# Optimization experiments

Hardware: AMD Instinct MI355X
Metric: run time of the kernel (lower is better)

## Reference

```python
import jax, jax.numpy as jnp
import numpy as np

B, L, D, NH, NP = 8, 4096, 384, 8, 4


def setup_inputs() -> dict:
    key = jax.random.key(0)
    ks = jax.random.split(key, 16)
    s = 1.0 / np.sqrt(D)
    f32 = jnp.float32
    inp = {
        'query': jax.random.normal(ks[0], (B, L, D), f32),
        'key':   jax.random.normal(ks[1], (B, L, D), f32),
        'value': jax.random.normal(ks[2], (B, L, D), f32),
        # linear weights stored as [in, out]; x @ W + b
        'Wq': jax.random.normal(ks[3], (D, D), f32) * s,
        'bq': jnp.zeros((D,), f32),
        'Wk': jax.random.normal(ks[4], (D, D), f32) * s,
        'bk': jnp.zeros((D,), f32),
        'Wv': jax.random.normal(ks[5], (D, D), f32) * s,
        'bv': jnp.zeros((D,), f32),
        'Woff': jax.random.normal(ks[6], (D, NH * NP * 2), f32) * s,
        'boff': jnp.zeros((NH * NP * 2,), f32),
        'Wwt': jax.random.normal(ks[7], (D, NH * NP), f32) * s,
        'bwt': jnp.zeros((NH * NP,), f32),
        'Wo': jax.random.normal(ks[8], (D, D), f32) * s,
        'bo': jnp.zeros((D,), f32),
        'num_heads': NH,
        'n_points': NP,
    }
    return inp


def reference(query, key, value, Wq, bq, Wk, bk, Wv, bv, Woff, boff, Wwt, bwt, Wo, bo, num_heads, n_points):
    Bq, Lq, Dm = query.shape
    Lk = key.shape[1]
    Lv = value.shape[1]
    hd = Dm // num_heads
    h = w = int(round(np.sqrt(Lk)))  # original: feature_size = int(sqrt(Lk))

    q = query @ Wq + bq          # computed as in original (only its reshape is used via output path)
    k = key @ Wk + bk            # faithful: k_proj is computed but unused downstream
    v = value @ Wv + bv

    # offsets [B, nH, Lq, nP, 2] and softmax point weights [B, nH, Lq, nP]
    off = (query @ Woff + boff).reshape(Bq, Lq, num_heads, n_points, 2).transpose(0, 2, 1, 3, 4)
    wt = jax.nn.softmax((query @ Wwt + bwt).reshape(Bq, Lq, num_heads, n_points).transpose(0, 2, 1, 3), axis=-1)

    # reference grid: ref[...,0] = x (tiled over rows), ref[...,1] = y (repeated over cols)
    yy = jnp.linspace(0.0, 1.0, h)
    xx = jnp.linspace(0.0, 1.0, w)
    gy, gx = jnp.meshgrid(yy, xx, indexing='ij')
    ref = jnp.stack([gx.reshape(-1), gy.reshape(-1)], axis=-1)  # [L, 2]

    loc = jnp.clip(ref[None, None, :, None, :] + off, 0.0, 1.0)  # [B,nH,Lq,nP,2]
    # NOTE: faithful to source, which multiplies component 0 by (h-1) (its 'h' coord)
    ph = loc[..., 0] * (h - 1)   # row pixel coord, in [0, h-1]
    pw = loc[..., 1] * (w - 1)   # col pixel coord, in [0, w-1]

    y0 = jnp.floor(ph)
    x0 = jnp.floor(pw)
    wy = (ph - y0)[..., None]
    wx = (pw - x0)[..., None]
    y0i = y0.astype(jnp.int32)
    x0i = x0.astype(jnp.int32)
    y1i = jnp.minimum(y0i + 1, h - 1)
    x1i = jnp.minimum(x0i + 1, w - 1)

    vh = v.reshape(Bq, Lv, num_heads, hd).transpose(0, 2, 1, 3)  # [B,nH,Lv,hd]

    def gather(yi, xi):
        idx = (yi * w + xi).reshape(Bq, num_heads, Lq * n_points, 1)
        return jnp.take_along_axis(vh, idx, axis=2).reshape(Bq, num_heads, Lq, n_points, hd)

    # bilinear sample (align_corners=True; coords in-range so zero-padding never triggers)
    sampled = ((1 - wy) * ((1 - wx) * gather(y0i, x0i) + wx * gather(y0i, x1i))
               + wy * ((1 - wx) * gather(y1i, x0i) + wx * gather(y1i, x1i)))

    out = jnp.einsum('bhlp,bhlpd->bhld', wt, sampled)  # weighted point aggregation
    out = out.transpose(0, 2, 1, 3).reshape(Bq, Lq, Dm)
    return out @ Wo + bo  # dropout is identity in eval mode
```

## Files before the change

### kernel.cpp

```cpp
#include <hip/hip_runtime.h>
#include <hip/hip_bf16.h>
#include <stdint.h>

using bf16 = __hip_bfloat16;

typedef __attribute__((ext_vector_type(8))) short short8;
typedef __attribute__((ext_vector_type(4))) float float4v;

namespace {
constexpr int kL  = 4096;
constexpr int kD  = 384;
constexpr int kGW = 64;
constexpr int kM  = 32768;
constexpr int kAP = 392;

constexpr size_t nValue = (size_t)kM * kD;
constexpr size_t nW     = (size_t)kD * kD;
constexpr size_t nWcat  = (size_t)96 * kD;

constexpr size_t oWvt  = 0;
constexpr size_t oWot  = oWvt  + nW * 2;
constexpr size_t oWch  = oWot  + nW * 2;
constexpr size_t oWcl  = oWch  + nWcat * 2;
constexpr size_t oBcat = oWcl  + nWcat * 2;
constexpr size_t oVB   = (oBcat + 96 * 4 + 255) & ~size_t(255);
constexpr size_t oProj = oVB   + nValue * 2;
}

__device__ __forceinline__ void load_lds_16(const void* g, void* l) {
  __builtin_amdgcn_global_load_lds((const __attribute__((address_space(1))) void*)g,
                                   (__attribute__((address_space(3))) void*)l,
                                   16, 0, 0);
}

__device__ __forceinline__ short bf16bits(float f) {
  bf16 h = __float2bfloat16(f);
  return *reinterpret_cast<short*>(&h);
}

__device__ __forceinline__ float bf16raw2f(unsigned short u) {
  union { unsigned int i; float f; } c;
  c.i = ((unsigned int)u) << 16;
  return c.f;
}

__device__ __forceinline__ short8 pack_hi8(const float4& f0, const float4& f1) {
  short8 hx;
  hx[0] = bf16bits(f0.x); hx[1] = bf16bits(f0.y);
  hx[2] = bf16bits(f0.z); hx[3] = bf16bits(f0.w);
  hx[4] = bf16bits(f1.x); hx[5] = bf16bits(f1.y);
  hx[6] = bf16bits(f1.z); hx[7] = bf16bits(f1.w);
  return hx;
}

__device__ __forceinline__ void pack_hilo8(const float4& f0, const float4& f1,
                                           short8& hx, short8& lx) {
  const float fv[8] = {f0.x, f0.y, f0.z, f0.w, f1.x, f1.y, f1.z, f1.w};
  #pragma unroll
  for (int q = 0; q < 8; ++q) {
    const bf16 h = __float2bfloat16(fv[q]);
    hx[q] = *reinterpret_cast<const short*>(&h);
    const bf16 lo = __float2bfloat16(fv[q] - __bfloat162float(h));
    lx[q] = *reinterpret_cast<const short*>(&lo);
  }
}

__global__ void prep_kernel(const float* __restrict__ Wv,
                            const float* __restrict__ Wo,
                            const float* __restrict__ Woff,
                            const float* __restrict__ Wwt,
                            const float* __restrict__ boff,
                            const float* __restrict__ bwt,
                            bf16* __restrict__ Wvt, bf16* __restrict__ Wot,
                            bf16* __restrict__ Wch, bf16* __restrict__ Wcl,
                            float* __restrict__ bcat)
{
  size_t i = (size_t)blockIdx.x * 256 + threadIdx.x;
  if (i < nW) {
    const int n = (int)(i / kD), k = (int)(i % kD);
    Wvt[i] = __float2bfloat16(Wv[(size_t)k * kD + n]);
    return;
  }
  i -= nW;
  if (i < nW) {
    const int n = (int)(i / kD), k = (int)(i % kD);
    Wot[i] = __float2bfloat16(Wo[(size_t)k * kD + n]);
    return;
  }
  i -= nW;
  if (i < nWcat) {
    const int n = (int)(i / kD), k = (int)(i % kD);
    const float val = (n < 64) ? Woff[(size_t)k * 64 + n] : Wwt[(size_t)k * 32 + (n - 64)];
    const bf16 h = __float2bfloat16(val);
    Wch[i] = h;
    Wcl[i] = __float2bfloat16(val - __bfloat162float(h));
    return;
  }
  i -= nWcat;
  if (i < 96) bcat[i] = (i < 64) ? boff[i] : bwt[i - 64];
}

__device__ __forceinline__
void vgemm_body(char* smem, int bid,
                const float* __restrict__ A, const bf16* __restrict__ Bt,
                const float* __restrict__ bias, bf16* __restrict__ Cout)
{
  bf16* sA = (bf16*)smem;
  char* sBB = smem + 16384;
  const int tid  = threadIdx.x;
  const int lane = tid & 63;
  const int wave = tid >> 6;
  const int bm = bid / 3, bn = bid % 3;
  const int m0 = bm * 128, n0 = bn * 128;
  const int wm = (wave >> 1) * 64, wn = (wave & 1) * 64;
  const int r16 = lane & 15, quad = lane >> 4;

  float4v acc[4][4];
  #pragma unroll
  for (int i = 0; i < 4; ++i)
    #pragma unroll
    for (int j = 0; j < 4; ++j) acc[i][j] = (float4v){0.f, 0.f, 0.f, 0.f};

  const int e0 = tid, e1 = tid + 256;
  const int rA0 = e0 >> 2, gA0 = e0 & 3;
  const int rA1 = e1 >> 2, gA1 = e1 & 3;
  const int wA0 = rA0 * 32 + (gA0 ^ ((rA0 >> 1) & 3)) * 8;
  const int wA1 = rA1 * 32 + (gA1 ^ ((rA1 >> 1) & 3)) * 8;
  const int sBc0 = (gA0 ^ ((rA0 >> 1) & 3)) * 8;
  const int sBc1 = (gA1 ^ ((rA1 >> 1) & 3)) * 8;

  float4 f00, f01, f10, f11;
  auto loadA = [&](int k0) {
    const float* s0 = A + (size_t)(m0 + rA0) * kD + k0 + gA0 * 8;
    f00 = *(const float4*)s0; f01 = *(const float4*)(s0 + 4);
    const float* s1 = A + (size_t)(m0 + rA1) * kD + k0 + gA1 * 8;
    f10 = *(const float4*)s1; f11 = *(const float4*)(s1 + 4);
  };
  auto writeA = [&](int buf) {
    *(short8*)(sA + buf * 4096 + wA0) = pack_hi8(f00, f01);
    *(short8*)(sA + buf * 4096 + wA1) = pack_hi8(f10, f11);
  };
  auto stageB = [&](int k0, int buf) {
    load_lds_16(Bt + (size_t)(n0 + rA0) * kD + k0 + sBc0, sBB + buf * 8192 + e0 * 16);
    load_lds_16(Bt + (size_t)(n0 + rA1) * kD + k0 + sBc1, sBB + buf * 8192 + e1 * 16);
  };

  loadA(0);
  stageB(0, 0);
  writeA(0);
  __syncthreads();

  for (int kt = 0; kt < 12; ++kt) {
    const int cur = kt & 1, nxt = cur ^ 1;
    if (kt < 11) {
      loadA((kt + 1) * 32);
      stageB((kt + 1) * 32, nxt);
    }
    const bf16* sAc = sA + cur * 4096;
    const bf16* sBc = (const bf16*)(sBB + cur * 8192);
    short8 av[4], bv[4];
    #pragma unroll
    for (int i = 0; i < 4; ++i) {
      const int row = wm + i * 16 + r16;
      av[i] = *(const short8*)(sAc + row * 32 + (quad ^ ((row >> 1) & 3)) * 8);
    }
    #pragma unroll
    for (int j = 0; j < 4; ++j) {
      const int row = wn + j * 16 + r16;
      bv[j] = *(const short8*)(sBc + row * 32 + (quad ^ ((row >> 1) & 3)) * 8);
    }
    #pragma unroll
    for (int i = 0; i < 4; ++i)
      #pragma unroll
      for (int j = 0; j < 4; ++j)
        acc[i][j] = __builtin_amdgcn_mfma_f32_16x16x32_bf16(av[i], bv[j], acc[i][j], 0, 0, 0);
    if (kt < 11) {
      writeA(nxt);
      __syncthreads();
    }
  }

  #pragma unroll
  for (int j = 0; j < 4; ++j) {
    const int col = n0 + wn + j * 16 + r16;
    const float bj = bias[col];
    #pragma unroll
    for (int i = 0; i < 4; ++i) {
      const int mbase = m0 + wm + i * 16 + quad * 4;
      #pragma unroll
      for (int r = 0; r < 4; ++r)
        Cout[(size_t)(mbase + r) * kD + col] = __float2bfloat16(acc[i][j][r] + bj);
    }
  }
}

__device__ __forceinline__
void proj_body(char* smem, int bid,
               const float* __restrict__ Q,
               const bf16* __restrict__ WhT, const bf16* __restrict__ WlT,
               const float* __restrict__ bc, float* __restrict__ proj)
{
  bf16* sAh = (bf16*)smem;
  bf16* sAl = (bf16*)(smem + 8192);
  bf16* sBh = (bf16*)(smem + 16384);
  bf16* sBl = (bf16*)(smem + 22528);
  const int tid  = threadIdx.x;
  const int lane = tid & 63;
  const int wave = tid >> 6;
  const int m0 = bid * 128;
  const int wm = (wave >> 1) * 64, wn = (wave & 1) * 48;
  const int r16 = lane & 15, quad = lane >> 4;

  float4v acc[4][3];
  #pragma unroll
  for (int i = 0; i < 4; ++i)
    #pragma unroll
    for (int j = 0; j < 3; ++j) acc[i][j] = (float4v){0.f, 0.f, 0.f, 0.f};

  for (int kt = 0; kt < 12; ++kt) {
    const int k0 = kt * 32;
    #pragma unroll
    for (int r = 0; r < 2; ++r) {
      const int e = tid + r * 256;
      const int row = e >> 2, j = e & 3;
      const float* src = Q + (size_t)(m0 + row) * kD + k0 + j * 8;
      const float4 f0 = *(const float4*)src;
      const float4 f1 = *(const float4*)(src + 4);
      short8 hx, lx;
      pack_hilo8(f0, f1, hx, lx);
      const int jw = j ^ ((row >> 1) & 3);
      *(short8*)(sAh + row * 32 + jw * 8) = hx;
      *(short8*)(sAl + row * 32 + jw * 8) = lx;
    }
    {
      int c = tid;
      int row = c >> 2, j = c & 3, js = j ^ ((row >> 1) & 3);
      load_lds_16(WhT + (size_t)row * kD + k0 + js * 8, (char*)sBh + c * 16);
      if (tid < 128) {
        c = tid + 256;
        row = c >> 2; j = c & 3; js = j ^ ((row >> 1) & 3);
        load_lds_16(WhT + (size_t)row * kD + k0 + js * 8, (char*)sBh + c * 16);
      } else {
        c = tid - 128;
        row = c >> 2; j = c & 3; js = j ^ ((row >> 1) & 3);
        load_lds_16(WlT + (size_t)row * kD + k0 + js * 8, (char*)sBl + c * 16);
      }
      c = tid + 128;
      row = c >> 2; j = c & 3; js = j ^ ((row >> 1) & 3);
      load_lds_16(WlT + (size_t)row * kD + k0 + js * 8, (char*)sBl + c * 16);
    }
    __syncthreads();

    short8 avh[4], avl[4];
    #pragma unroll
    for (int i = 0; i < 4; ++i) {
      const int row = wm + i * 16 + r16;
      const int ch = quad ^ ((row >> 1) & 3);
      avh[i] = *(const short8*)(sAh + row * 32 + ch * 8);
      avl[i] = *(const short8*)(sAl + row * 32 + ch * 8);
    }
    #pragma unroll
    for (int j = 0; j < 3; ++j) {
      const int row = wn + j * 16 + r16;
      const int ch = quad ^ ((row >> 1) & 3);
      const short8 bvh = *(const short8*)(sBh + row * 32 + ch * 8);
      const short8 bvl = *(const short8*)(sBl + row * 32 + ch * 8);
      #pragma unroll
      for (int i = 0; i < 4; ++i) {
        acc[i][j] = __builtin_amdgcn_mfma_f32_16x16x32_bf16(avh[i], bvh, acc[i][j], 0, 0, 0);
        acc[i][j] = __builtin_amdgcn_mfma_f32_16x16x32_bf16(avh[i], bvl, acc[i][j], 0, 0, 0);
        acc[i][j] = __builtin_amdgcn_mfma_f32_16x16x32_bf16(avl[i], bvh, acc[i][j], 0, 0, 0);
      }
    }
    __syncthreads();
  }

  #pragma unroll
  for (int j = 0; j < 3; ++j) {
    const int col = wn + j * 16 + r16;
    const float bj = bc[col];
    #pragma unroll
    for (int i = 0; i < 4; ++i) {
      const int mbase = m0 + wm + i * 16 + quad * 4;
      #pragma unroll
      for (int r = 0; r < 4; ++r)
        proj[(size_t)(mbase + r) * 96 + col] = acc[i][j][r] + bj;
    }
  }
}

__global__ __launch_bounds__(256)
void fat_kernel(const float* __restrict__ value, const bf16* __restrict__ Wvt,
                const float* __restrict__ bv,    bf16* __restrict__ vB,
                const float* __restrict__ Q,     const bf16* __restrict__ Wch,
                const bf16* __restrict__ Wcl,    const float* __restrict__ bcat,
                float* __restrict__ proj)
{
  __shared__ __align__(16) char smem[32768];
  const int pb = blockIdx.x;
  if (pb < 256) {
    proj_body(smem, pb, Q, Wch, Wcl, bcat, proj);
  } else {
    vgemm_body(smem, pb - 256, value, Wvt, bv, vB);
  }
}

__global__ __launch_bounds__(512)
void tail_kernel(const float* __restrict__ proj, const bf16* __restrict__ v,
                 const bf16* __restrict__ Wot, const float* __restrict__ bo,
                 float* __restrict__ out)
{
  __shared__ __align__(16) char smem[66560];
  bf16*   sAgg  = (bf16*)smem;
  int4*   scoff = (int4*)(smem + 50176);
  float4* scw   = (float4*)(smem + 58368);

  const int raw   = blockIdx.x;
  const int chunk = (raw & 7) * 64 + (raw >> 3);
  const int m0    = chunk * 64;
  const int b     = m0 >> 12;
  const int l0    = m0 & 4095;
  const int t     = threadIdx.x;

  for (int ct = 0; ct < 4; ++ct) {
    const int tok0 = ct * 16;
    {
      const int tl = t >> 5, pt = t & 31;
      const int tok = tok0 + tl;
      const int l   = l0 + tok;
      const float* pb_ = proj + (size_t)(m0 + tok) * 96;
      const float2 off = *(const float2*)(pb_ + 2 * pt);
      const int h = pt >> 2, p = pt & 3;
      const float4 lg = *(const float4*)(pb_ + 64 + h * 4);
      const float g[4] = {lg.x, lg.y, lg.z, lg.w};
      const float mx = fmaxf(fmaxf(g[0], g[1]), fmaxf(g[2], g[3]));
      float e[4], sum = 0.f;
      #pragma unroll
      for (int jj = 0; jj < 4; ++jj) { e[jj] = expf(g[jj] - mx); sum += e[jj]; }
      const float wt = e[p] / sum;
      const float refx = (float)(l & 63) * (1.0f / 63.0f);
      const float refy = (float)(l >> 6) * (1.0f / 63.0f);
      const float locx = fminf(fmaxf(refx + off.x, 0.f), 1.f);
      const float locy = fminf(fmaxf(refy + off.y, 0.f), 1.f);
      const float ph = locx * 63.0f;
      const float pw = locy * 63.0f;
      const float fy = floorf(ph), fx = floorf(pw);
      const int y0 = (int)fy, x0 = (int)fx;
      const int y1 = min(y0 + 1, 63), x1 = min(x0 + 1, 63);
      const float wy = ph - fy, wx = pw - fx;
      scoff[tl * 32 + pt] = make_int4((y0 * kGW + x0) * kD, (y0 * kGW + x1) * kD,
                                      (y1 * kGW + x0) * kD, (y1 * kGW + x1) * kD);
      scw[tl * 32 + pt] = make_float4(wt * (1.f - wy) * (1.f - wx), wt * (1.f - wy) * wx,
                                      wt * wy * (1.f - wx),         wt * wy * wx);
    }
    __syncthreads();
    #pragma unroll
    for (int it = 0; it < 3; ++it) {
      const int task = t + it * 512;
      const int tl = task / 96;
      const int q  = task - tl * 96;
      const int h  = q / 12;
      const int col = q * 4;
      const unsigned short* vb = (const unsigned short*)(v + (size_t)b * kL * kD + col);
      float4v acc = (float4v){0.f, 0.f, 0.f, 0.f};
      #pragma unroll
      for (int p = 0; p < 4; ++p) {
        const int4   o = scoff[tl * 32 + h * 4 + p];
        const float4 w = scw  [tl * 32 + h * 4 + p];
        const ushort4 u0 = *(const ushort4*)(vb + o.x);
        const ushort4 u1 = *(const ushort4*)(vb + o.y);
        const ushort4 u2 = *(const ushort4*)(vb + o.z);
        const ushort4 u3 = *(const ushort4*)(vb + o.w);
        acc[0] += w.x * bf16raw2f(u0.x) + w.y * bf16raw2f(u1.x)
                + w.z * bf16raw2f(u2.x) + w.w * bf16raw2f(u3.x);
        acc[1] += w.x * bf16raw2f(u0.y) + w.y * bf16raw2f(u1.y)
                + w.z * bf16raw2f(u2.y) + w.w * bf16raw2f(u3.y);
        acc[2] += w.x * bf16raw2f(u0.z) + w.y * bf16raw2f(u1.z)
                + w.z * bf16raw2f(u2.z) + w.w * bf16raw2f(u3.z);
        acc[3] += w.x * bf16raw2f(u0.w) + w.y * bf16raw2f(u1.w)
                + w.z * bf16raw2f(u2.w) + w.w * bf16raw2f(u3.w);
      }
      ushort4 ou;
      ou.x = (unsigned short)bf16bits(acc[0]);
      ou.y = (unsigned short)bf16bits(acc[1]);
      ou.z = (unsigned short)bf16bits(acc[2]);
      ou.w = (unsigned short)bf16bits(acc[3]);
      *(ushort4*)(sAgg + (size_t)(tok0 + tl) * kAP + col) = ou;
    }
    __syncthreads();
  }

  const int lane = t & 63, wave = t >> 6;
  const int r16 = lane & 15, quad = lane >> 4;
  const int wn = wave * 48;
  float4v acc2[4][3];
  #pragma unroll
  for (int i = 0; i < 4; ++i)
    #pragma unroll
    for (int j = 0; j < 3; ++j) acc2[i][j] = (float4v){0.f, 0.f, 0.f, 0.f};

  const bf16* Bbase = Wot + (size_t)(wn + r16) * kD + quad * 8;

  #pragma unroll
  for (int kt = 0; kt < 12; ++kt) {
    const int k0 = kt * 32;
    short8 av[4];
    #pragma unroll
    for (int i = 0; i < 4; ++i)
      av[i] = *(const short8*)(sAgg + (size_t)(i * 16 + r16) * kAP + k0 + quad * 8);
    #pragma unroll
    for (int j = 0; j < 3; ++j) {
      const short8 bvj = *(const short8*)(Bbase + (size_t)(j * 16) * kD + k0);
      #pragma unroll
      for (int i = 0; i < 4; ++i)
        acc2[i][j] = __builtin_amdgcn_mfma_f32_16x16x32_bf16(av[i], bvj, acc2[i][j], 0, 0, 0);
    }
  }

  #pragma unroll
  for (int j = 0; j < 3; ++j) {
    const int col = wn + j * 16 + r16;
    const float bj = bo[col];
    #pragma unroll
    for (int i = 0; i < 4; ++i) {
      const int mb = m0 + i * 16 + quad * 4;
      #pragma unroll
      for (int r = 0; r < 4; ++r)
        out[(size_t)(mb + r) * kD + col] = acc2[i][j][r] + bj;
    }
  }
}

extern "C" void kernel_launch(void* const* d_in, const int* in_sizes, int n_in,
                              void* d_out, int out_size, void* d_ws, size_t ws_size,
                              hipStream_t stream)
{
  const float* query = (const float*)d_in[0];
  const float* value = (const float*)d_in[2];
  const float* Wv    = (const float*)d_in[7];
  const float* bv    = (const float*)d_in[8];
  const float* Woff  = (const float*)d_in[9];
  const float* boff  = (const float*)d_in[10];
  const float* Wwt   = (const float*)d_in[11];
  const float* bwt   = (const float*)d_in[12];
  const float* Wo    = (const float*)d_in[13];
  const float* bo    = (const float*)d_in[14];
  float* out = (float*)d_out;

  char* ws = (char*)d_ws;
  bf16*  Wvt  = (bf16*)(ws + oWvt);
  bf16*  Wot  = (bf16*)(ws + oWot);
  bf16*  Wch  = (bf16*)(ws + oWch);
  bf16*  Wcl  = (bf16*)(ws + oWcl);
  float* bcat = (float*)(ws + oBcat);
  bf16*  vB   = (bf16*)(ws + oVB);
  float* proj = (float*)(ws + oProj);

  const size_t prepN = nW + nW + nWcat + 96;
  prep_kernel<<<dim3((unsigned)((prepN + 255) / 256)), 256, 0, stream>>>(
      Wv, Wo, Woff, Wwt, boff, bwt, Wvt, Wot, Wch, Wcl, bcat);

  fat_kernel<<<dim3(256 + 768), 256, 0, stream>>>(
      value, Wvt, bv, vB, query, Wch, Wcl, bcat, proj);

  tail_kernel<<<dim3(512), 512, 0, stream>>>(proj, vB, Wot, bo, out);
}
```

Measured before the change: 264.9 us.

## Halve GEMM M-tiles, double-buffer proj loads, remap vgemm blocks, widen gather vectors

```diff
diff --git a/kernel.cpp b/kernel.cpp
--- a/kernel.cpp
+++ b/kernel.cpp
@@ -106,43 +106,40 @@
                 const float* __restrict__ bias, bf16* __restrict__ Cout)
 {
   bf16* sA = (bf16*)smem;
-  char* sBB = smem + 16384;
+  char* sBB = smem + 8192;
   const int tid  = threadIdx.x;
   const int lane = tid & 63;
   const int wave = tid >> 6;
   const int bm = bid / 3, bn = bid % 3;
-  const int m0 = bm * 128, n0 = bn * 128;
-  const int wm = (wave >> 1) * 64, wn = (wave & 1) * 64;
+  const int m0 = bm * 64, n0 = bn * 128;
+  const int wm = (wave >> 1) * 32, wn = (wave & 1) * 64;
   const int r16 = lane & 15, quad = lane >> 4;
 
-  float4v acc[4][4];
-  #pragma unroll
-  for (int i = 0; i < 4; ++i)
+  float4v acc[2][4];
+  #pragma unroll
+  for (int i = 0; i < 2; ++i)
     #pragma unroll
     for (int j = 0; j < 4; ++j) acc[i][j] = (float4v){0.f, 0.f, 0.f, 0.f};
 
+  const int rA = tid >> 2, gA = tid & 3;
+  const int wA = rA * 32 + (gA ^ ((rA >> 1) & 3)) * 8;
   const int e0 = tid, e1 = tid + 256;
-  const int rA0 = e0 >> 2, gA0 = e0 & 3;
-  const int rA1 = e1 >> 2, gA1 = e1 & 3;
-  const int wA0 = rA0 * 32 + (gA0 ^ ((rA0 >> 1) & 3)) * 8;
-  const int wA1 = rA1 * 32 + (gA1 ^ ((rA1 >> 1) & 3)) * 8;
-  const int sBc0 = (gA0 ^ ((rA0 >> 1) & 3)) * 8;
-  const int sBc1 = (gA1 ^ ((rA1 >> 1) & 3)) * 8;
-
-  float4 f00, f01, f10, f11;
+  const int rB0 = e0 >> 2, gB0 = e0 & 3;
+  const int rB1 = e1 >> 2, gB1 = e1 & 3;
+  const int sBc0 = (gB0 ^ ((rB0 >> 1) & 3)) * 8;
+  const int sBc1 = (gB1 ^ ((rB1 >> 1) & 3)) * 8;
+
+  float4 f00, f01;
   auto loadA = [&](int k0) {
-    const float* s0 = A + (size_t)(m0 + rA0) * kD + k0 + gA0 * 8;
+    const float* s0 = A + (size_t)(m0 + rA) * kD + k0 + gA * 8;
     f00 = *(const float4*)s0; f01 = *(const float4*)(s0 + 4);
-    const float* s1 = A + (size_t)(m0 + rA1) * kD + k0 + gA1 * 8;
-    f10 = *(const float4*)s1; f11 = *(const float4*)(s1 + 4);
   };
   auto writeA = [&](int buf) {
-    *(short8*)(sA + buf * 4096 + wA0) = pack_hi8(f00, f01);
-    *(short8*)(sA + buf * 4096 + wA1) = pack_hi8(f10, f11);
+    *(short8*)(sA + buf * 2048 + wA) = pack_hi8(f00, f01);
   };
   auto stageB = [&](int k0, int buf) {
-    load_lds_16(Bt + (size_t)(n0 + rA0) * kD + k0 + sBc0, sBB + buf * 8192 + e0 * 16);
-    load_lds_16(Bt + (size_t)(n0 + rA1) * kD + k0 + sBc1, sBB + buf * 8192 + e1 * 16);
+    load_lds_16(Bt + (size_t)(n0 + rB0) * kD + k0 + sBc0, sBB + buf * 8192 + e0 * 16);
+    load_lds_16(Bt + (size_t)(n0 + rB1) * kD + k0 + sBc1, sBB + buf * 8192 + e1 * 16);
   };
 
   loadA(0);
@@ -156,11 +153,11 @@
       loadA((kt + 1) * 32);
       stageB((kt + 1) * 32, nxt);
     }
-    const bf16* sAc = sA + cur * 4096;
+    const bf16* sAc = sA + cur * 2048;
     const bf16* sBc = (const bf16*)(sBB + cur * 8192);
-    short8 av[4], bv[4];
-    #pragma unroll
-    for (int i = 0; i < 4; ++i) {
+    short8 av[2], bv[4];
+    #pragma unroll
+    for (int i = 0; i < 2; ++i) {
       const int row = wm + i * 16 + r16;
       av[i] = *(const short8*)(sAc + row * 32 + (quad ^ ((row >> 1) & 3)) * 8);
     }
@@ -170,7 +167,7 @@
       bv[j] = *(const short8*)(sBc + row * 32 + (quad ^ ((row >> 1) & 3)) * 8);
     }
     #pragma unroll
-    for (int i = 0; i < 4; ++i)
+    for (int i = 0; i < 2; ++i)
       #pragma unroll
       for (int j = 0; j < 4; ++j)
         acc[i][j] = __builtin_amdgcn_mfma_f32_16x16x32_bf16(av[i], bv[j], acc[i][j], 0, 0, 0);
@@ -185,7 +182,7 @@
     const int col = n0 + wn + j * 16 + r16;
     const float bj = bias[col];
     #pragma unroll
-    for (int i = 0; i < 4; ++i) {
+    for (int i = 0; i < 2; ++i) {
       const int mbase = m0 + wm + i * 16 + quad * 4;
       #pragma unroll
       for (int r = 0; r < 4; ++r)
@@ -201,59 +198,65 @@
                const float* __restrict__ bc, float* __restrict__ proj)
 {
   bf16* sAh = (bf16*)smem;
-  bf16* sAl = (bf16*)(smem + 8192);
-  bf16* sBh = (bf16*)(smem + 16384);
-  bf16* sBl = (bf16*)(smem + 22528);
+  bf16* sAl = (bf16*)(smem + 4096);
+  bf16* sBh = (bf16*)(smem + 8192);
+  bf16* sBl = (bf16*)(smem + 14336);
   const int tid  = threadIdx.x;
   const int lane = tid & 63;
   const int wave = tid >> 6;
-  const int m0 = bid * 128;
-  const int wm = (wave >> 1) * 64, wn = (wave & 1) * 48;
+  const int m0 = bid * 64;
+  const int wm = (wave >> 1) * 32, wn = (wave & 1) * 48;
   const int r16 = lane & 15, quad = lane >> 4;
 
-  float4v acc[4][3];
-  #pragma unroll
-  for (int i = 0; i < 4; ++i)
+  float4v acc[2][3];
+  #pragma unroll
+  for (int i = 0; i < 2; ++i)
     #pragma unroll
     for (int j = 0; j < 3; ++j) acc[i][j] = (float4v){0.f, 0.f, 0.f, 0.f};
 
-  for (int kt = 0; kt < 12; ++kt) {
-    const int k0 = kt * 32;
-    #pragma unroll
-    for (int r = 0; r < 2; ++r) {
-      const int e = tid + r * 256;
-      const int row = e >> 2, j = e & 3;
-      const float* src = Q + (size_t)(m0 + row) * kD + k0 + j * 8;
-      const float4 f0 = *(const float4*)src;
-      const float4 f1 = *(const float4*)(src + 4);
-      short8 hx, lx;
-      pack_hilo8(f0, f1, hx, lx);
-      const int jw = j ^ ((row >> 1) & 3);
-      *(short8*)(sAh + row * 32 + jw * 8) = hx;
-      *(short8*)(sAl + row * 32 + jw * 8) = lx;
-    }
-    {
-      int c = tid;
-      int row = c >> 2, j = c & 3, js = j ^ ((row >> 1) & 3);
+  const int rA = tid >> 2, gA = tid & 3;
+  const int jwA = (gA ^ ((rA >> 1) & 3));
+
+  float4 f0, f1;
+  auto loadA = [&](int k0) {
+    const float* src = Q + (size_t)(m0 + rA) * kD + k0 + gA * 8;
+    f0 = *(const float4*)src; f1 = *(const float4*)(src + 4);
+  };
+  auto writeA = [&]() {
+    short8 hx, lx;
+    pack_hilo8(f0, f1, hx, lx);
+    *(short8*)(sAh + rA * 32 + jwA * 8) = hx;
+    *(short8*)(sAl + rA * 32 + jwA * 8) = lx;
+  };
+  auto stageB = [&](int k0) {
+    int c = tid;
+    int row = c >> 2, j = c & 3, js = j ^ ((row >> 1) & 3);
+    load_lds_16(WhT + (size_t)row * kD + k0 + js * 8, (char*)sBh + c * 16);
+    if (tid < 128) {
+      c = tid + 256;
+      row = c >> 2; j = c & 3; js = j ^ ((row >> 1) & 3);
       load_lds_16(WhT + (size_t)row * kD + k0 + js * 8, (char*)sBh + c * 16);
-      if (tid < 128) {
-        c = tid + 256;
-        row = c >> 2; j = c & 3; js = j ^ ((row >> 1) & 3);
-        load_lds_16(WhT + (size_t)row * kD + k0 + js * 8, (char*)sBh + c * 16);
-      } else {
-        c = tid - 128;
-        row = c >> 2; j = c & 3; js = j ^ ((row >> 1) & 3);
-        load_lds_16(WlT + (size_t)row * kD + k0 + js * 8, (char*)sBl + c * 16);
-      }
-      c = tid + 128;
+    } else {
+      c = tid - 128;
       row = c >> 2; j = c & 3; js = j ^ ((row >> 1) & 3);
       load_lds_16(WlT + (size_t)row * kD + k0 + js * 8, (char*)sBl + c * 16);
     }
-    __syncthreads();
-
-    short8 avh[4], avl[4];
-    #pragma unroll
-    for (int i = 0; i < 4; ++i) {
+    c = tid + 128;
+    row = c >> 2; j = c & 3; js = j ^ ((row >> 1) & 3);
+    load_lds_16(WlT + (size_t)row * kD + k0 + js * 8, (char*)sBl + c * 16);
+  };
+
+  loadA(0);
+  stageB(0);
+  writeA();
+  __syncthreads();
+
+  for (int kt = 0; kt < 12; ++kt) {
+    if (kt < 11) loadA((kt + 1) * 32);
+
+    short8 avh[2], avl[2];
+    #pragma unroll
+    for (int i = 0; i < 2; ++i) {
       const int row = wm + i * 16 + r16;
       const int ch = quad ^ ((row >> 1) & 3);
       avh[i] = *(const short8*)(sAh + row * 32 + ch * 8);
@@ -266,13 +269,18 @@
       const short8 bvh = *(const short8*)(sBh + row * 32 + ch * 8);
       const short8 bvl = *(const short8*)(sBl + row * 32 + ch * 8);
       #pragma unroll
-      for (int i = 0; i < 4; ++i) {
+      for (int i = 0; i < 2; ++i) {
         acc[i][j] = __builtin_amdgcn_mfma_f32_16x16x32_bf16(avh[i], bvh, acc[i][j], 0, 0, 0);
         acc[i][j] = __builtin_amdgcn_mfma_f32_16x16x32_bf16(avh[i], bvl, acc[i][j], 0, 0, 0);
         acc[i][j] = __builtin_amdgcn_mfma_f32_16x16x32_bf16(avl[i], bvh, acc[i][j], 0, 0, 0);
       }
     }
-    __syncthreads();
+    if (kt < 11) {
+      __syncthreads();
+      stageB((kt + 1) * 32);
+      writeA();
+      __syncthreads();
+    }
   }
 
   #pragma unroll
@@ -280,7 +288,7 @@
     const int col = wn + j * 16 + r16;
     const float bj = bc[col];
     #pragma unroll
-    for (int i = 0; i < 4; ++i) {
+    for (int i = 0; i < 2; ++i) {
       const int mbase = m0 + wm + i * 16 + quad * 4;
       #pragma unroll
       for (int r = 0; r < 4; ++r)
@@ -296,12 +304,14 @@
                 const bf16* __restrict__ Wcl,    const float* __restrict__ bcat,
                 float* __restrict__ proj)
 {
-  __shared__ __align__(16) char smem[32768];
+  __shared__ __align__(16) char smem[24576];
   const int pb = blockIdx.x;
-  if (pb < 256) {
+  if (pb < 512) {
     proj_body(smem, pb, Q, Wch, Wcl, bcat, proj);
   } else {
-    vgemm_body(smem, pb - 256, value, Wvt, bv, vB);
+    const int vb   = pb - 512;
+    const int wgid = (vb & 7) * 192 + (vb >> 3);
+    vgemm_body(smem, wgid, value, Wvt, bv, vB);
   }
 }
 
@@ -355,37 +365,36 @@
     }
     __syncthreads();
     #pragma unroll
-    for (int it = 0; it < 3; ++it) {
+    for (int it = 0; it < 2; ++it) {
       const int task = t + it * 512;
-      const int tl = task / 96;
-      const int q  = task - tl * 96;
-      const int h  = q / 12;
-      const int col = q * 4;
-      const unsigned short* vb = (const unsigned short*)(v + (size_t)b * kL * kD + col);
-      float4v acc = (float4v){0.f, 0.f, 0.f, 0.f};
-      #pragma unroll
-      for (int p = 0; p < 4; ++p) {
-        const int4   o = scoff[tl * 32 + h * 4 + p];
-        const float4 w = scw  [tl * 32 + h * 4 + p];
-        const ushort4 u0 = *(const ushort4*)(vb + o.x);
-        const ushort4 u1 = *(const ushort4*)(vb + o.y);
-        const ushort4 u2 = *(const ushort4*)(vb + o.z);
-        const ushort4 u3 = *(const ushort4*)(vb + o.w);
-        acc[0] += w.x * bf16raw2f(u0.x) + w.y * bf16raw2f(u1.x)
-                + w.z * bf16raw2f(u2.x) + w.w * bf16raw2f(u3.x);
-        acc[1] += w.x * bf16raw2f(u0.y) + w.y * bf16raw2f(u1.y)
-                + w.z * bf16raw2f(u2.y) + w.w * bf16raw2f(u3.y);
-        acc[2] += w.x * bf16raw2f(u0.z) + w.y * bf16raw2f(u1.z)
-                + w.z * bf16raw2f(u2.z) + w.w * bf16raw2f(u3.z);
-        acc[3] += w.x * bf16raw2f(u0.w) + w.y * bf16raw2f(u1.w)
-                + w.z * bf16raw2f(u2.w) + w.w * bf16raw2f(u3.w);
+      if (task < 768) {
+        const int tl = task / 48;
+        const int g  = task - tl * 48;
+        const int h  = g / 6;
+        const int col = g * 8;
+        const bf16* vb = v + (size_t)b * kL * kD + col;
+        float av[8] = {0.f, 0.f, 0.f, 0.f, 0.f, 0.f, 0.f, 0.f};
+        #pragma unroll
+        for (int p = 0; p < 4; ++p) {
+          const int4   o = scoff[tl * 32 + h * 4 + p];
+          const float4 w = scw  [tl * 32 + h * 4 + p];
+          const short8 u0 = *(const short8*)(vb + o.x);
+          const short8 u1 = *(const short8*)(vb + o.y);
+          const short8 u2 = *(const short8*)(vb + o.z);
+          const short8 u3 = *(const short8*)(vb + o.w);
+          #pragma unroll
+          for (int d = 0; d < 8; ++d) {
+            av[d] += w.x * bf16raw2f((unsigned short)u0[d])
+                   + w.y * bf16raw2f((unsigned short)u1[d])
+                   + w.z * bf16raw2f((unsigned short)u2[d])
+                   + w.w * bf16raw2f((unsigned short)u3[d]);
+          }
+        }
+        short8 ou;
+        #pragma unroll
+        for (int d = 0; d < 8; ++d) ou[d] = bf16bits(av[d]);
+        *(short8*)(sAgg + (size_t)(tok0 + tl) * kAP + col) = ou;
       }
-      ushort4 ou;
-      ou.x = (unsigned short)bf16bits(acc[0]);
-      ou.y = (unsigned short)bf16bits(acc[1]);
-      ou.z = (unsigned short)bf16bits(acc[2]);
-      ou.w = (unsigned short)bf16bits(acc[3]);
-      *(ushort4*)(sAgg + (size_t)(tok0 + tl) * kAP + col) = ou;
     }
     __syncthreads();
   }
@@ -460,7 +469,7 @@
   prep_kernel<<<dim3((unsigned)((prepN + 255) / 256)), 256, 0, stream>>>(
       Wv, Wo, Woff, Wwt, boff, bwt, Wvt, Wot, Wch, Wcl, bcat);
 
-  fat_kernel<<<dim3(256 + 768), 256, 0, stream>>>(
+  fat_kernel<<<dim3(512 + 1536), 256, 0, stream>>>(
       value, Wvt, bv, vB, query, Wch, Wcl, bcat, proj);
 
   tail_kernel<<<dim3(512), 512, 0, stream>>>(proj, vB, Wot, bo, out);
```

After: 263.6 us. No clear change (-0.5%).
